# Kernel optimization log

Measured on AMD Instinct MI355X. Metric: run time of the kernel, lower is better.

Reference implementation:

```python
import jax, jax.numpy as jnp
import numpy as np

CH_IN = 256
CH_OUT = 32


def setup_inputs() -> dict:
    key = jax.random.key(0)
    ks = jax.random.split(key, 7)
    b, c, H, W = 4, CH_IN, 64, 64
    x = jax.random.normal(ks[0], (b, c, H, W), dtype=jnp.float32)
    # 1x1 conv weights (out, in) and biases, small init like torch default
    sc_in = 1.0 / np.sqrt(CH_IN)
    Wf = jax.random.uniform(ks[1], (CH_OUT, CH_IN), jnp.float32, -sc_in, sc_in)
    bf = jax.random.uniform(ks[2], (CH_OUT,), jnp.float32, -sc_in, sc_in)
    Wg = jax.random.uniform(ks[3], (CH_OUT, CH_IN), jnp.float32, -sc_in, sc_in)
    bg = jax.random.uniform(ks[4], (CH_OUT,), jnp.float32, -sc_in, sc_in)
    Wh = jax.random.uniform(ks[5], (CH_IN, CH_IN), jnp.float32, -sc_in, sc_in)
    bh = jax.random.uniform(ks[6], (CH_IN,), jnp.float32, -sc_in, sc_in)
    return {"x": x, "Wf": Wf, "bf": bf, "Wg": Wg, "bg": bg, "Wh": Wh, "bh": bh}


def reference(x, Wf, bf, Wg, bg, Wh, bh):
    b, c, H, W = x.shape
    xf = x.reshape(b, c, H * W)                      # [b, c, N]
    # 1x1 convs == per-pixel linear projections
    f = jnp.einsum('oc,bcn->bon', Wf, xf) + bf[None, :, None]   # [b, ch_out, N]
    g = jnp.einsum('oc,bcn->bon', Wg, xf) + bg[None, :, None]   # [b, ch_out, N]
    h = jnp.einsum('oc,bcn->bon', Wh, xf) + bh[None, :, None]   # [b, ch_in, N]
    # s[b, i, j] = sum_o f[b,o,i] * g[b,o,j]
    s = jnp.einsum('boi,boj->bij', f, g)             # [b, N, N]
    # torch softmax over dim=1 (the i axis)
    beta = jax.nn.softmax(s, axis=1)                 # [b, N, N]
    # o = h @ beta : [b, c, N] x [b, N, N] -> [b, c, N]
    o = jnp.einsum('bcn,bnm->bcm', h, beta)
    return o.reshape(b, c, H, W)
```

## Files before the change

kernel.cpp:

```cpp
#include <hip/hip_runtime.h>
#include <hip/hip_bf16.h>
#include <math.h>

#define BATCH 4
#define CIN   256
#define DQK   32
#define NPIX  4096
#define MTOT  320

typedef __attribute__((ext_vector_type(4))) float f32x4;
typedef __attribute__((ext_vector_type(8))) short bf16x8;
typedef __attribute__((ext_vector_type(4))) unsigned int u32x4;

__device__ __forceinline__ unsigned short f2bf(float f) {
  unsigned u = __builtin_bit_cast(unsigned, f);
  u += 0x7FFFu + ((u >> 16) & 1u);
  return (unsigned short)(u >> 16);
}
__device__ __forceinline__ unsigned pk2(float a, float b) {
  return (unsigned)f2bf(a) | ((unsigned)f2bf(b) << 16);
}
__device__ __forceinline__ void barrier_lds() {
  asm volatile("s_waitcnt lgkmcnt(0)" ::: "memory");
  __builtin_amdgcn_s_barrier();
  asm volatile("" ::: "memory");
}
__device__ __forceinline__ void wait_vm4_lgkm0() { asm volatile("s_waitcnt vmcnt(4) lgkmcnt(0)" ::: "memory"); }
__device__ __forceinline__ void wait_vm5_lgkm0() { asm volatile("s_waitcnt vmcnt(5) lgkmcnt(0)" ::: "memory"); }

#define GLD16(GP, LP) \
  __builtin_amdgcn_global_load_lds((const __attribute__((address_space(1))) void*)(GP), \
                                   (__attribute__((address_space(3))) void*)(LP), 16, 0, 0)

__global__ void wcvt(const float* __restrict__ Wh, const float* __restrict__ Wf,
                     const float* __restrict__ Wg,
                     const float* __restrict__ bh, const float* __restrict__ bf,
                     const float* __restrict__ bg,
                     unsigned short* __restrict__ Wb, float* __restrict__ bcat) {
  const int r = blockIdx.x;
  const int c = threadIdx.x;
  const float* src = (r < 256) ? &Wh[r * CIN] : (r < 288) ? &Wf[(r - 256) * CIN] : &Wg[(r - 288) * CIN];
  Wb[r * CIN + c] = f2bf(src[c]);
  if (c == 0)
    bcat[r] = (r < 256) ? bh[r] : (r < 288) ? bf[r - 256] : bg[r - 288];
}

#define XPAD 4
__launch_bounds__(512, 1)
__global__ void proj_all(const float* __restrict__ x, const unsigned short* __restrict__ Wb,
                         const float* __restrict__ bcat,
                         unsigned short* __restrict__ F, unsigned short* __restrict__ G,
                         unsigned short* __restrict__ H) {
  __shared__ unsigned short Xs[64 * (CIN + XPAD)];

  const int bid = blockIdx.x;
  const int b = bid >> 6;
  const int n0 = (bid & 63) << 6;
  const int t = threadIdx.x;
  const int lane = t & 63;
  const int w = t >> 6;

  const float* __restrict__ xb = x + (size_t)b * CIN * NPIX + n0;
#pragma unroll
  for (int p = 0; p < 16; ++p) {
    const int k = p * 16 + w * 2;
    const float a0 = xb[(size_t)k * NPIX + lane];
    const float a1 = xb[(size_t)(k + 1) * NPIX + lane];
    const unsigned pk = (unsigned)f2bf(a0) | ((unsigned)f2bf(a1) << 16);
    *(unsigned*)((char*)Xs + lane * (CIN + XPAD) * 2 + k * 2) = pk;
  }
  __syncthreads();

  const int l16 = lane & 15, lhi = lane >> 4;
  const int wm = w >> 1;
  const int wn = w & 1;

  const f32x4 fzero = {0.f, 0.f, 0.f, 0.f};
  f32x4 acc[5][2];
#pragma unroll
  for (int i = 0; i < 5; ++i)
#pragma unroll
    for (int j = 0; j < 2; ++j) acc[i][j] = fzero;

#pragma unroll
  for (int ks = 0; ks < 8; ++ks) {
    bf16x8 bx[2];
#pragma unroll
    for (int j = 0; j < 2; ++j)
      bx[j] = *(const bf16x8*)&Xs[(wn * 32 + j * 16 + l16) * (CIN + XPAD) + ks * 32 + lhi * 8];
#pragma unroll
    for (int i = 0; i < 5; ++i) {
      const bf16x8 aw = *(const bf16x8*)(Wb + (size_t)(wm * 80 + i * 16 + l16) * CIN + ks * 32 + lhi * 8);
#pragma unroll
      for (int j = 0; j < 2; ++j)
        acc[i][j] = __builtin_amdgcn_mfma_f32_16x16x32_bf16(aw, bx[j], acc[i][j], 0, 0, 0);
    }
  }

#pragma unroll
  for (int i = 0; i < 5; ++i) {
    const int MT = wm * 5 + i;
    const int m0 = MT * 16;
    const f32x4 bias = *(const f32x4*)&bcat[m0 + lhi * 4];
#pragma unroll
    for (int j = 0; j < 2; ++j) {
      const int n = n0 + wn * 32 + j * 16 + l16;
      f32x4 v = acc[i][j];
      v.x += bias.x; v.y += bias.y; v.z += bias.z; v.w += bias.w;
      if (MT < 16) {
        const int c0 = m0 + lhi * 4;
        unsigned short* dst = H + ((size_t)b * CIN + c0) * NPIX + n;
        dst[0 * NPIX] = f2bf(v.x);
        dst[1 * NPIX] = f2bf(v.y);
        dst[2 * NPIX] = f2bf(v.z);
        dst[3 * NPIX] = f2bf(v.w);
      } else {
        unsigned short* dst = (MT < 18) ? F : G;
        const int d0 = ((MT - 16) & 1) * 16 + lhi * 4;
        uint2 pk;
        pk.x = (unsigned)f2bf(v.x) | ((unsigned)f2bf(v.y) << 16);
        pk.y = (unsigned)f2bf(v.z) | ((unsigned)f2bf(v.w) << 16);
        *(uint2*)(dst + ((size_t)b * NPIX + n) * DQK + d0) = pk;
      }
    }
  }
}

#define BNK  64
#define KEYS 2048
#define NTILE (KEYS / BNK)

__launch_bounds__(512, 1)
__global__ void attn_split(const unsigned short* __restrict__ F,
                           const unsigned short* __restrict__ G,
                           const unsigned short* __restrict__ H,
                           unsigned short* __restrict__ Ap, float* __restrict__ Lp) {
  __shared__ unsigned short Kl[3][64][32];
  __shared__ unsigned short Vl[3][256][64];
  __shared__ unsigned short Pl[2][2][64][72];

  const int bid = blockIdx.x;
  const int slab = bid & 7;
  const int b = slab >> 1;
  const int split = slab & 1;
  const int qt = bid >> 3;
  const int t = threadIdx.x;
  const int lane = t & 63, w = t >> 6;
  const int l16 = lane & 15, lhi = lane >> 4;
  const int mg = w >> 2, cs = w & 3;

  const unsigned short* Fb = F + (size_t)b * NPIX * DQK;
  const unsigned short* Gb = G + (size_t)b * NPIX * DQK;
  const unsigned short* Hb = H + (size_t)b * CIN * NPIX;
  const int nb0 = split * KEYS;
  const int q0 = qt * 128 + mg * 64;

  const f32x4 fzero = {0.f, 0.f, 0.f, 0.f};

  bf16x8 qf[4];
#pragma unroll
  for (int mt = 0; mt < 4; ++mt)
    qf[mt] = *(const bf16x8*)(Gb + (size_t)(q0 + mt * 16 + l16) * DQK + lhi * 8);

  f32x4 acc[4][4];
#pragma unroll
  for (int ct = 0; ct < 4; ++ct)
#pragma unroll
    for (int mt = 0; mt < 4; ++mt) acc[ct][mt] = fzero;
  float Lacc[4] = {0.f, 0.f, 0.f, 0.f};

  const char* vsrc = (const char*)Hb + ((size_t)(8 * w + (lane >> 3)) * NPIX + nb0) * 2
                   + (((lane & 7) ^ (lane >> 3)) * 16);
  const int kw = (w >= 4) ? (w - 4) : 0;
  const char* ksrc = (const char*)Fb + ((size_t)(nb0 + 16 * kw + (lane >> 2)) * DQK) * 2
                   + (((lane & 3) ^ ((lane >> 2) & 3)) * 16);

#define ISSUE(TT) do {                                                           \
    const int bu_ = (TT) % 3;                                                    \
    _Pragma("unroll")                                                            \
    for (int i_ = 0; i_ < 4; ++i_)                                               \
      GLD16(vsrc + (size_t)i_ * 64 * NPIX * 2 + (size_t)(TT) * 128,              \
            &Vl[bu_][i_ * 64 + 8 * w][0]);                                       \
    if (w >= 4)                                                                  \
      GLD16(ksrc + (size_t)(TT) * 64 * DQK * 2, &Kl[bu_][16 * kw][0]);           \
  } while (0)

#define BSTART() do {                                                            \
    if (w >= 4) wait_vm5_lgkm0(); else wait_vm4_lgkm0();                         \
    __builtin_amdgcn_s_barrier();                                                \
    asm volatile("" ::: "memory");                                               \
  } while (0)

#define QKSM(BUF3, PAR) do {                                                     \
    const unsigned short* kb_ = &Kl[BUF3][0][0];                                 \
    const bf16x8 kf_ = *(const bf16x8*)(kb_ + (cs * 16 + l16) * 32 + ((lhi ^ (l16 & 3)) * 8)); \
    f32x4 s_[4];                                                                 \
    _Pragma("unroll")                                                            \
    for (int mt_ = 0; mt_ < 4; ++mt_)                                            \
      s_[mt_] = __builtin_amdgcn_mfma_f32_16x16x32_bf16(kf_, qf[mt_], fzero, 0, 0, 0); \
    _Pragma("unroll")                                                            \
    for (int mt_ = 0; mt_ < 4; ++mt_) {                                          \
      const float p0 = __expf(s_[mt_][0]), p1 = __expf(s_[mt_][1]);              \
      const float p2 = __expf(s_[mt_][2]), p3 = __expf(s_[mt_][3]);              \
      Lacc[mt_] += (p0 + p1) + (p2 + p3);                                        \
      uint2 pk_; pk_.x = pk2(p0, p1); pk_.y = pk2(p2, p3);                       \
      *(uint2*)&Pl[PAR][mg][mt_ * 16 + l16][cs * 16 + lhi * 4] = pk_;            \
    }                                                                            \
  } while (0)

#define PVACC(BUF3, PF) do {                                                     \
    const unsigned short* vb_ = &Vl[BUF3][0][0];                                 \
    __builtin_amdgcn_s_setprio(1);                                               \
    _Pragma("unroll")                                                            \
    for (int kk_ = 0; kk_ < 2; ++kk_)                                            \
      _Pragma("unroll")                                                          \
      for (int ct_ = 0; ct_ < 4; ++ct_) {                                        \
        const bf16x8 vf_ = *(const bf16x8*)(vb_ + (cs * 64 + ct_ * 16 + l16) * 64 \
                            + (((4 * kk_ + lhi) ^ (l16 & 7)) * 8));              \
        _Pragma("unroll")                                                        \
        for (int mt_ = 0; mt_ < 4; ++mt_)                                        \
          acc[ct_][mt_] = __builtin_amdgcn_mfma_f32_16x16x32_bf16(vf_, PF[mt_][kk_], acc[ct_][mt_], 0, 0, 0); \
      }                                                                          \
    __builtin_amdgcn_s_setprio(0);                                               \
  } while (0)

  ISSUE(0); ISSUE(1); ISSUE(2);
  BSTART();
  QKSM(0, 0);

  for (int tt = 0; tt < NTILE; ++tt) {
    const int par = tt & 1;
    BSTART();
    bf16x8 pf[4][2];
#pragma unroll
    for (int mt = 0; mt < 4; ++mt)
#pragma unroll
      for (int kk = 0; kk < 2; ++kk)
        pf[mt][kk] = *(const bf16x8*)&Pl[par][mg][mt * 16 + l16][kk * 32 + lhi * 8];
    if (tt + 1 < NTILE) QKSM((tt + 1) % 3, par ^ 1);
    PVACC(tt % 3, pf);
    barrier_lds();
    if (tt + 3 < NTILE) ISSUE(tt + 3);
  }
#undef ISSUE
#undef BSTART
#undef QKSM
#undef PVACC

#pragma unroll
  for (int mt = 0; mt < 4; ++mt) {
    float L = Lacc[mt];
    L += __shfl_xor(L, 16, 64);
    L += __shfl_xor(L, 32, 64);
    if (lhi == 0)
      Lp[((size_t)split * 4 + cs) * (4 * NPIX) + (size_t)b * NPIX + q0 + mt * 16 + l16] = L;
  }
#pragma unroll
  for (int ct = 0; ct < 4; ++ct)
#pragma unroll
    for (int mt = 0; mt < 4; ++mt) {
      const int c = cs * 64 + ct * 16 + lhi * 4;
      const int q = q0 + mt * 16 + l16;
      unsigned short* dst = Ap + (((size_t)split * 4 + b) * CIN + c) * NPIX + q;
#pragma unroll
      for (int v = 0; v < 4; ++v) dst[(size_t)v * NPIX] = f2bf(acc[ct][mt][v]);
    }
}

__global__ void combineL(const float* __restrict__ Lp, float* __restrict__ Linv) {
  const int idx = blockIdx.x * 256 + threadIdx.x;
  float s = 0.f;
#pragma unroll
  for (int i = 0; i < 8; ++i) s += Lp[(size_t)i * (4 * NPIX) + idx];
  Linv[idx] = 1.f / s;
}

__global__ void combine(const unsigned short* __restrict__ Ap, const float* __restrict__ Linv,
                        float* __restrict__ out) {
  const size_t base = ((size_t)blockIdx.x * 256 + threadIdx.x) * 8;
  const int b = (int)(base / ((size_t)CIN * NPIX));
  const int q = (int)(base % NPIX);
  const u32x4 a0 = *(const u32x4*)(Ap + base);
  const u32x4 a1 = *(const u32x4*)(Ap + (size_t)4 * CIN * NPIX + base);
  const float* lv = &Linv[(size_t)b * NPIX + q];
  float r[8];
#pragma unroll
  for (int i = 0; i < 4; ++i) {
    const float x0 = __builtin_bit_cast(float, (a0[i] & 0xFFFFu) << 16) +
                     __builtin_bit_cast(float, (a1[i] & 0xFFFFu) << 16);
    const float x1 = __builtin_bit_cast(float, (a0[i] & 0xFFFF0000u)) +
                     __builtin_bit_cast(float, (a1[i] & 0xFFFF0000u));
    r[2 * i] = x0 * lv[2 * i];
    r[2 * i + 1] = x1 * lv[2 * i + 1];
  }
  *(f32x4*)&out[base] = *(f32x4*)&r[0];
  *(f32x4*)&out[base + 4] = *(f32x4*)&r[4];
}

#define BN 32
__launch_bounds__(512, 2)
__global__ void attn_kernel(const unsigned short* __restrict__ F,
                            const unsigned short* __restrict__ G,
                            const unsigned short* __restrict__ H,
                            float* __restrict__ out) {
  __shared__ unsigned short Klds[32 * 40];
  __shared__ unsigned short Vlds[256 * 40];
  __shared__ unsigned short Plds[8][32 * 40];

  const int bid = blockIdx.x;
  const int b = bid >> 6;
  const int t = threadIdx.x;
  const int lane = t & 63;
  const int w = t >> 6;
  const int l16 = lane & 15;
  const int lhi = lane >> 4;
  const int m0 = ((bid & 63) << 6) + ((w >> 2) << 5);
  const int c0 = (w & 3) << 6;

  const f32x4 fzero = {0.f, 0.f, 0.f, 0.f};

  bf16x8 qf[2];
#pragma unroll
  for (int mt = 0; mt < 2; ++mt)
    qf[mt] = *(const bf16x8*)(G + ((size_t)b * NPIX + m0 + mt * 16 + l16) * DQK + lhi * 8);

  f32x4 acc[4][2];
#pragma unroll
  for (int ct = 0; ct < 4; ++ct)
#pragma unroll
    for (int mt = 0; mt < 2; ++mt) acc[ct][mt] = fzero;
  float Mr[2] = {-INFINITY, -INFINITY};
  float Lr[2] = {0.f, 0.f};

  const unsigned short* Fb = F + (size_t)b * NPIX * DQK;
  const unsigned short* Hb = H + (size_t)b * CIN * NPIX;
  unsigned short* Pw = &Plds[w][0];

  for (int n0 = 0; n0 < NPIX; n0 += BN) {
    __syncthreads();
    if (t < 128) {
      const int nr = t >> 2, sl = t & 3;
      *(u32x4*)&Klds[nr * 40 + sl * 8] = *(const u32x4*)(Fb + (size_t)(n0 + nr) * DQK + sl * 8);
    }
#pragma unroll
    for (int i = 0; i < 2; ++i) {
      const int q = t + i * 512;
      const int cr = q >> 2, sl = q & 3;
      *(u32x4*)&Vlds[cr * 40 + sl * 8] = *(const u32x4*)(Hb + (size_t)cr * NPIX + n0 + sl * 8);
    }
    __syncthreads();

    bf16x8 kf[2];
#pragma unroll
    for (int nts = 0; nts < 2; ++nts)
      kf[nts] = *(const bf16x8*)&Klds[(nts * 16 + l16) * 40 + lhi * 8];
    f32x4 s[2][2];
#pragma unroll
    for (int mt = 0; mt < 2; ++mt)
#pragma unroll
      for (int nts = 0; nts < 2; ++nts)
        s[mt][nts] = __builtin_amdgcn_mfma_f32_16x16x32_bf16(kf[nts], qf[mt], fzero, 0, 0, 0);

#pragma unroll
    for (int mt = 0; mt < 2; ++mt) {
      float tmax = s[mt][0][0];
#pragma unroll
      for (int v = 1; v < 4; ++v) tmax = fmaxf(tmax, s[mt][0][v]);
#pragma unroll
      for (int v = 0; v < 4; ++v) tmax = fmaxf(tmax, s[mt][1][v]);
      tmax = fmaxf(tmax, __shfl_xor(tmax, 16, 64));
      tmax = fmaxf(tmax, __shfl_xor(tmax, 32, 64));
      const float newM = fmaxf(Mr[mt], tmax);
      const float rescale = __expf(Mr[mt] - newM);
      Mr[mt] = newM;
      float p[2][4];
      float psum = 0.f;
#pragma unroll
      for (int nts = 0; nts < 2; ++nts)
#pragma unroll
        for (int v = 0; v < 4; ++v) {
          p[nts][v] = __expf(s[mt][nts][v] - newM);
          psum += p[nts][v];
        }
      psum += __shfl_xor(psum, 16, 64);
      psum += __shfl_xor(psum, 32, 64);
      Lr[mt] = Lr[mt] * rescale + psum;
#pragma unroll
      for (int ct = 0; ct < 4; ++ct) acc[ct][mt] *= rescale;
#pragma unroll
      for (int nts = 0; nts < 2; ++nts) {
        uint2 pkv;
        pkv.x = (unsigned)f2bf(p[nts][0]) | ((unsigned)f2bf(p[nts][1]) << 16);
        pkv.y = (unsigned)f2bf(p[nts][2]) | ((unsigned)f2bf(p[nts][3]) << 16);
        *(uint2*)&Pw[(mt * 16 + l16) * 40 + nts * 16 + lhi * 4] = pkv;
      }
    }
    asm volatile("" ::: "memory");

    bf16x8 pf[2];
#pragma unroll
    for (int mt = 0; mt < 2; ++mt)
      pf[mt] = *(const bf16x8*)&Pw[(mt * 16 + l16) * 40 + lhi * 8];
#pragma unroll
    for (int ct = 0; ct < 4; ++ct) {
      const bf16x8 vf = *(const bf16x8*)&Vlds[(c0 + ct * 16 + l16) * 40 + lhi * 8];
#pragma unroll
      for (int mt = 0; mt < 2; ++mt)
        acc[ct][mt] = __builtin_amdgcn_mfma_f32_16x16x32_bf16(vf, pf[mt], acc[ct][mt], 0, 0, 0);
    }
  }

#pragma unroll
  for (int mt = 0; mt < 2; ++mt) {
    const float invL = 1.f / Lr[mt];
    const int m = m0 + mt * 16 + l16;
#pragma unroll
    for (int ct = 0; ct < 4; ++ct)
#pragma unroll
      for (int v = 0; v < 4; ++v) {
        const int c = c0 + ct * 16 + lhi * 4 + v;
        out[((size_t)b * CIN + c) * NPIX + m] = acc[ct][mt][v] * invL;
      }
  }
}

extern "C" void kernel_launch(void* const* d_in, const int* in_sizes, int n_in,
                              void* d_out, int out_size, void* d_ws, size_t ws_size,
                              hipStream_t stream) {
  (void)in_sizes; (void)n_in; (void)out_size;
  const float* x  = (const float*)d_in[0];
  const float* Wf = (const float*)d_in[1];
  const float* bf = (const float*)d_in[2];
  const float* Wg = (const float*)d_in[3];
  const float* bg = (const float*)d_in[4];
  const float* Wh = (const float*)d_in[5];
  const float* bh = (const float*)d_in[6];
  float* out = (float*)d_out;

  unsigned short* Fw = (unsigned short*)d_ws;
  unsigned short* Gw = Fw + (size_t)BATCH * NPIX * DQK;
  unsigned short* Hw = Gw + (size_t)BATCH * NPIX * DQK;
  unsigned short* Wb = Hw + (size_t)BATCH * CIN * NPIX;
  float* bcat = (float*)(Wb + (size_t)MTOT * CIN);
  unsigned short* Apart = (unsigned short*)(bcat + MTOT);
  float* Lpart = (float*)(Apart + (size_t)2 * BATCH * CIN * NPIX);
  float* Linv  = Lpart + (size_t)8 * BATCH * NPIX;
  const size_t NEED = (size_t)((char*)(Linv + (size_t)BATCH * NPIX) - (char*)d_ws);

  hipLaunchKernelGGL(wcvt, dim3(MTOT), dim3(256), 0, stream, Wh, Wf, Wg, bh, bf, bg, Wb, bcat);
  hipLaunchKernelGGL(proj_all, dim3(BATCH * 64), dim3(512), 0, stream, x, Wb, bcat, Fw, Gw, Hw);

  if (ws_size >= NEED) {
    hipLaunchKernelGGL(attn_split, dim3(BATCH * 32 * 2), dim3(512), 0, stream, Fw, Gw, Hw, Apart, Lpart);
    hipLaunchKernelGGL(combineL, dim3(BATCH * NPIX / 256), dim3(256), 0, stream, Lpart, Linv);
    hipLaunchKernelGGL(combine, dim3((size_t)BATCH * CIN * NPIX / 8 / 256), dim3(256), 0, stream, Apart, Linv, out);
  } else {
    hipLaunchKernelGGL(attn_kernel, dim3(BATCH * 64), dim3(512), 0, stream, Fw, Gw, Hw, out);
  }
}
```

Measured before the change: 87.99 us.

## Restructure split attention to per-wave query tiles with P kept in registers

Each wave now owns 16 queries and all 256 channels instead of splitting 64 queries across channel slices. The exp(S) tile therefore stays in registers and feeds 16x16x16 MFMAs directly, which removes the P staging buffer in LDS and its barrier. The pipeline drops to double-issue prefetch with one barrier per tile, and launch bounds now allow two blocks per CU. The cost is more V reads from LDS per wave, since each wave reads the whole V tile, and the smaller-K MFMA variant.

New measurement: 117.4 us. 1.33x slower.

```diff
diff --git a/kernel.cpp b/kernel.cpp
--- a/kernel.cpp
+++ b/kernel.cpp
@@ -10,6 +10,7 @@
 
 typedef __attribute__((ext_vector_type(4))) float f32x4;
 typedef __attribute__((ext_vector_type(8))) short bf16x8;
+typedef __attribute__((ext_vector_type(4))) short bf16x4;
 typedef __attribute__((ext_vector_type(4))) unsigned int u32x4;
 
 __device__ __forceinline__ unsigned short f2bf(float f) {
@@ -27,6 +28,7 @@
 }
 __device__ __forceinline__ void wait_vm4_lgkm0() { asm volatile("s_waitcnt vmcnt(4) lgkmcnt(0)" ::: "memory"); }
 __device__ __forceinline__ void wait_vm5_lgkm0() { asm volatile("s_waitcnt vmcnt(5) lgkmcnt(0)" ::: "memory"); }
+__device__ __forceinline__ void wait_vm0_lgkm0() { asm volatile("s_waitcnt vmcnt(0) lgkmcnt(0)" ::: "memory"); }
 
 #define GLD16(GP, LP) \
   __builtin_amdgcn_global_load_lds((const __attribute__((address_space(1))) void*)(GP), \
@@ -130,14 +132,13 @@
 #define KEYS 2048
 #define NTILE (KEYS / BNK)
 
-__launch_bounds__(512, 1)
+__launch_bounds__(512, 2)
 __global__ void attn_split(const unsigned short* __restrict__ F,
                            const unsigned short* __restrict__ G,
                            const unsigned short* __restrict__ H,
                            unsigned short* __restrict__ Ap, float* __restrict__ Lp) {
   __shared__ unsigned short Kl[3][64][32];
   __shared__ unsigned short Vl[3][256][64];
-  __shared__ unsigned short Pl[2][2][64][72];
 
   const int bid = blockIdx.x;
   const int slab = bid & 7;
@@ -147,27 +148,21 @@
   const int t = threadIdx.x;
   const int lane = t & 63, w = t >> 6;
   const int l16 = lane & 15, lhi = lane >> 4;
-  const int mg = w >> 2, cs = w & 3;
 
   const unsigned short* Fb = F + (size_t)b * NPIX * DQK;
   const unsigned short* Gb = G + (size_t)b * NPIX * DQK;
   const unsigned short* Hb = H + (size_t)b * CIN * NPIX;
   const int nb0 = split * KEYS;
-  const int q0 = qt * 128 + mg * 64;
+  const int qw = qt * 128 + w * 16;
 
   const f32x4 fzero = {0.f, 0.f, 0.f, 0.f};
 
-  bf16x8 qf[4];
-#pragma unroll
-  for (int mt = 0; mt < 4; ++mt)
-    qf[mt] = *(const bf16x8*)(Gb + (size_t)(q0 + mt * 16 + l16) * DQK + lhi * 8);
-
-  f32x4 acc[4][4];
-#pragma unroll
-  for (int ct = 0; ct < 4; ++ct)
-#pragma unroll
-    for (int mt = 0; mt < 4; ++mt) acc[ct][mt] = fzero;
-  float Lacc[4] = {0.f, 0.f, 0.f, 0.f};
+  const bf16x8 qf = *(const bf16x8*)(Gb + (size_t)(qw + l16) * DQK + lhi * 8);
+
+  f32x4 acc[16];
+#pragma unroll
+  for (int ct = 0; ct < 16; ++ct) acc[ct] = fzero;
+  float Lacc = 0.f;
 
   const char* vsrc = (const char*)Hb + ((size_t)(8 * w + (lane >> 3)) * NPIX + nb0) * 2
                    + (((lane & 7) ^ (lane >> 3)) * 16);
@@ -185,94 +180,69 @@
       GLD16(ksrc + (size_t)(TT) * 64 * DQK * 2, &Kl[bu_][16 * kw][0]);           \
   } while (0)
 
-#define BSTART() do {                                                            \
-    if (w >= 4) wait_vm5_lgkm0(); else wait_vm4_lgkm0();                         \
-    __builtin_amdgcn_s_barrier();                                                \
-    asm volatile("" ::: "memory");                                               \
-  } while (0)
-
-#define QKSM(BUF3, PAR) do {                                                     \
-    const unsigned short* kb_ = &Kl[BUF3][0][0];                                 \
-    const bf16x8 kf_ = *(const bf16x8*)(kb_ + (cs * 16 + l16) * 32 + ((lhi ^ (l16 & 3)) * 8)); \
-    f32x4 s_[4];                                                                 \
-    _Pragma("unroll")                                                            \
-    for (int mt_ = 0; mt_ < 4; ++mt_)                                            \
-      s_[mt_] = __builtin_amdgcn_mfma_f32_16x16x32_bf16(kf_, qf[mt_], fzero, 0, 0, 0); \
-    _Pragma("unroll")                                                            \
-    for (int mt_ = 0; mt_ < 4; ++mt_) {                                          \
-      const float p0 = __expf(s_[mt_][0]), p1 = __expf(s_[mt_][1]);              \
-      const float p2 = __expf(s_[mt_][2]), p3 = __expf(s_[mt_][3]);              \
-      Lacc[mt_] += (p0 + p1) + (p2 + p3);                                        \
-      uint2 pk_; pk_.x = pk2(p0, p1); pk_.y = pk2(p2, p3);                       \
-      *(uint2*)&Pl[PAR][mg][mt_ * 16 + l16][cs * 16 + lhi * 4] = pk_;            \
-    }                                                                            \
-  } while (0)
-
-#define PVACC(BUF3, PF) do {                                                     \
-    const unsigned short* vb_ = &Vl[BUF3][0][0];                                 \
-    __builtin_amdgcn_s_setprio(1);                                               \
-    _Pragma("unroll")                                                            \
-    for (int kk_ = 0; kk_ < 2; ++kk_)                                            \
-      _Pragma("unroll")                                                          \
-      for (int ct_ = 0; ct_ < 4; ++ct_) {                                        \
-        const bf16x8 vf_ = *(const bf16x8*)(vb_ + (cs * 64 + ct_ * 16 + l16) * 64 \
-                            + (((4 * kk_ + lhi) ^ (l16 & 7)) * 8));              \
-        _Pragma("unroll")                                                        \
-        for (int mt_ = 0; mt_ < 4; ++mt_)                                        \
-          acc[ct_][mt_] = __builtin_amdgcn_mfma_f32_16x16x32_bf16(vf_, PF[mt_][kk_], acc[ct_][mt_], 0, 0, 0); \
-      }                                                                          \
-    __builtin_amdgcn_s_setprio(0);                                               \
-  } while (0)
-
-  ISSUE(0); ISSUE(1); ISSUE(2);
-  BSTART();
-  QKSM(0, 0);
+  ISSUE(0); ISSUE(1);
 
   for (int tt = 0; tt < NTILE; ++tt) {
-    const int par = tt & 1;
-    BSTART();
-    bf16x8 pf[4][2];
-#pragma unroll
-    for (int mt = 0; mt < 4; ++mt)
-#pragma unroll
-      for (int kk = 0; kk < 2; ++kk)
-        pf[mt][kk] = *(const bf16x8*)&Pl[par][mg][mt * 16 + l16][kk * 32 + lhi * 8];
-    if (tt + 1 < NTILE) QKSM((tt + 1) % 3, par ^ 1);
-    PVACC(tt % 3, pf);
-    barrier_lds();
-    if (tt + 3 < NTILE) ISSUE(tt + 3);
+    const int bu = tt % 3;
+    if (tt + 1 < NTILE) { if (w >= 4) wait_vm5_lgkm0(); else wait_vm4_lgkm0(); }
+    else wait_vm0_lgkm0();
+    __builtin_amdgcn_s_barrier();
+    asm volatile("" ::: "memory");
+    if (tt + 2 < NTILE) ISSUE(tt + 2);
+
+    unsigned pkv[4][2];
+#pragma unroll
+    for (int nts = 0; nts < 4; ++nts) {
+      const bf16x8 kf = *(const bf16x8*)((const char*)&Kl[bu][nts * 16 + l16][0]
+                                         + ((lhi ^ (l16 & 3)) << 4));
+      const f32x4 s = __builtin_amdgcn_mfma_f32_16x16x32_bf16(kf, qf, fzero, 0, 0, 0);
+      const float p0 = __expf(s[0]), p1 = __expf(s[1]);
+      const float p2 = __expf(s[2]), p3 = __expf(s[3]);
+      Lacc += (p0 + p1) + (p2 + p3);
+      pkv[nts][0] = pk2(p0, p1);
+      pkv[nts][1] = pk2(p2, p3);
+    }
+    bf16x4 pf16[4];
+#pragma unroll
+    for (int nts = 0; nts < 4; ++nts) {
+      uint2 u; u.x = pkv[nts][0]; u.y = pkv[nts][1];
+      pf16[nts] = __builtin_bit_cast(bf16x4, u);
+    }
+
+    __builtin_amdgcn_s_setprio(1);
+#pragma unroll
+    for (int ct = 0; ct < 16; ++ct) {
+      const char* vrow = (const char*)&Vl[bu][ct * 16 + l16][0];
+      const int r7 = l16 & 7;
+#pragma unroll
+      for (int nts = 0; nts < 4; ++nts) {
+        const int s16 = (nts * 2 + (lhi >> 1)) ^ r7;
+        const bf16x4 vf = *(const bf16x4*)(vrow + (s16 << 4) + ((lhi & 1) << 3));
+        acc[ct] = __builtin_amdgcn_mfma_f32_16x16x16bf16_1k(vf, pf16[nts], acc[ct], 0, 0, 0);
+      }
+    }
+    __builtin_amdgcn_s_setprio(0);
   }
 #undef ISSUE
-#undef BSTART
-#undef QKSM
-#undef PVACC
-
-#pragma unroll
-  for (int mt = 0; mt < 4; ++mt) {
-    float L = Lacc[mt];
-    L += __shfl_xor(L, 16, 64);
-    L += __shfl_xor(L, 32, 64);
-    if (lhi == 0)
-      Lp[((size_t)split * 4 + cs) * (4 * NPIX) + (size_t)b * NPIX + q0 + mt * 16 + l16] = L;
-  }
-#pragma unroll
-  for (int ct = 0; ct < 4; ++ct)
-#pragma unroll
-    for (int mt = 0; mt < 4; ++mt) {
-      const int c = cs * 64 + ct * 16 + lhi * 4;
-      const int q = q0 + mt * 16 + l16;
-      unsigned short* dst = Ap + (((size_t)split * 4 + b) * CIN + c) * NPIX + q;
-#pragma unroll
-      for (int v = 0; v < 4; ++v) dst[(size_t)v * NPIX] = f2bf(acc[ct][mt][v]);
-    }
+
+  float L = Lacc;
+  L += __shfl_xor(L, 16, 64);
+  L += __shfl_xor(L, 32, 64);
+  const int q = qw + l16;
+  if (lhi == 0)
+    Lp[(size_t)split * (4 * NPIX) + (size_t)b * NPIX + q] = L;
+#pragma unroll
+  for (int ct = 0; ct < 16; ++ct) {
+    const int c = ct * 16 + lhi * 4;
+    unsigned short* dst = Ap + (((size_t)split * 4 + b) * CIN + c) * NPIX + q;
+#pragma unroll
+    for (int v = 0; v < 4; ++v) dst[(size_t)v * NPIX] = f2bf(acc[ct][v]);
+  }
 }
 
 __global__ void combineL(const float* __restrict__ Lp, float* __restrict__ Linv) {
   const int idx = blockIdx.x * 256 + threadIdx.x;
-  float s = 0.f;
-#pragma unroll
-  for (int i = 0; i < 8; ++i) s += Lp[(size_t)i * (4 * NPIX) + idx];
-  Linv[idx] = 1.f / s;
+  Linv[idx] = 1.f / (Lp[idx] + Lp[(size_t)4 * NPIX + idx]);
 }
 
 __global__ void combine(const unsigned short* __restrict__ Ap, const float* __restrict__ Linv,
@@ -444,7 +414,7 @@
   float* bcat = (float*)(Wb + (size_t)MTOT * CIN);
   unsigned short* Apart = (unsigned short*)(bcat + MTOT);
   float* Lpart = (float*)(Apart + (size_t)2 * BATCH * CIN * NPIX);
-  float* Linv  = Lpart + (size_t)8 * BATCH * NPIX;
+  float* Linv  = Lpart + (size_t)2 * 4 * NPIX;
   const size_t NEED = (size_t)((char*)(Linv + (size_t)BATCH * NPIX) - (char*)d_ws);
 
   hipLaunchKernelGGL(wcvt, dim3(MTOT), dim3(256), 0, stream, Wh, Wf, Wg, bh, bf, bg, Wb, bcat);
```
